# Kernel optimization log

Hardware: AMD Instinct MI355X
Metric: run time of the kernel (lower is better)

Reference implementation:

```python
import jax, jax.numpy as jnp
import numpy as np

B = 262144
N_HEADS = 30  # sum_{n=1..4} n^2
D_SHARED1, D_SHARED2, D_HEAD = 128, 64, 32


def setup_inputs() -> dict:
    key = jax.random.key(0)
    ks = jax.random.split(key, 12)
    x = jax.random.normal(ks[0], (B, 2), dtype=jnp.float32)
    # quantum numbers with validity constraints: 1<=n<=4, 0<=l<n, -l<=m<=l
    n = jax.random.randint(ks[1], (B,), 1, 5, dtype=jnp.int32)
    u1 = jax.random.uniform(ks[2], (B,))
    l = jnp.minimum(jnp.floor(u1 * n).astype(jnp.int32), n - 1)
    u2 = jax.random.uniform(ks[3], (B,))
    m = jnp.clip(jnp.floor(u2 * (2 * l + 1)).astype(jnp.int32) - l, -l, l)
    # shared MLP params (torch Linear -> y = x @ W + b with W stored [in,out] here)
    def xavier(k, shape):
        fan_in, fan_out = shape[-2], shape[-1]
        lim = np.sqrt(6.0 / (fan_in + fan_out)).astype(np.float32)
        return jax.random.uniform(k, shape, jnp.float32, -lim, lim)
    W1s = xavier(ks[4], (2, D_SHARED1))
    b1s = jnp.zeros((D_SHARED1,), jnp.float32)
    W2s = xavier(ks[5], (D_SHARED1, D_SHARED2))
    b2s = jnp.zeros((D_SHARED2,), jnp.float32)
    # stacked expert head params, flat head index = (n-1)n(2n-1)/6 + l^2 + (m+l)
    HW1 = xavier(ks[6], (N_HEADS, D_SHARED2, D_HEAD))
    Hb1 = jnp.zeros((N_HEADS, D_HEAD), jnp.float32)
    HW2 = xavier(ks[7], (N_HEADS, D_HEAD, 2))
    Hb2 = jnp.zeros((N_HEADS, 2), jnp.float32)
    return dict(x=x, n=n, l=l, m=m, W1s=W1s, b1s=b1s, W2s=W2s, b2s=b2s,
                HW1=HW1, Hb1=Hb1, HW2=HW2, Hb2=Hb2)


def reference(x, n, l, m, W1s, b1s, W2s, b2s, HW1, Hb1, HW2, Hb2):
    # shared MLP (dropout is identity in eval mode)
    h = jnp.tanh(x @ W1s + b1s)          # [B,128]
    h = jnp.tanh(h @ W2s + b2s)          # [B,64]
    # flat head id: cumulative squares offset + l^2 + (m+l)
    hid = (n - 1) * n * (2 * n - 1) // 6 + l * l + (m + l)   # [B] in [0,30)
    # per-sample dispatched tiny MLP via gathered weights (grouped batched matvec)
    z = jnp.tanh(jnp.einsum('bi,bio->bo', h, HW1[hid]) + Hb1[hid])   # [B,32]
    out = jnp.einsum('bi,bio->bo', z, HW2[hid]) + Hb2[hid]           # [B,2]
    return out  # [:,0] real part, [:,1] imag part
```

## Files before the change

kernel.cpp:

```cpp
#include <hip/hip_runtime.h>
#include <hip/hip_bf16.h>
#include <math.h>

#define B_TOTAL 262144
#define NHEADS  30
#define D1      128
#define D2      64
#define DH      32
#define BLK     256
#define NBLK_IN (B_TOTAL / BLK)
#define SB      128
#define MAX_MB  (B_TOTAL / SB + NHEADS)

#define TANH_K  2.885390081777927f

typedef __attribute__((ext_vector_type(8))) __bf16 bf16x8;
typedef __attribute__((ext_vector_type(4))) float  f32x4;


__device__ __forceinline__ int head_id(int nn, int ll, int mm) {
    return (nn - 1) * nn * (2 * nn - 1) / 6 + ll * ll + (mm + ll);
}

__device__ __forceinline__ float tanh_pre(float u) {
    float e = __builtin_amdgcn_exp2f(u);
    return 1.0f - 2.0f * __builtin_amdgcn_rcpf(e + 1.0f);
}

__global__ __launch_bounds__(BLK) void k_hist(const int* __restrict__ n,
                                              const int* __restrict__ l,
                                              const int* __restrict__ m,
                                              unsigned* __restrict__ block_counts,
                                              unsigned char* __restrict__ hids,
                                              const float* __restrict__ W2,
                                              const float* __restrict__ HW1,
                                              __bf16* __restrict__ W2f,
                                              __bf16* __restrict__ HW1f) {
    __shared__ unsigned lh[NHEADS];
    int t = threadIdx.x;
    if (t < NHEADS) lh[t] = 0u;
    __syncthreads();
    int i = blockIdx.x * BLK + t;
    int hid = head_id(n[i], l[i], m[i]);
    hids[i] = (unsigned char)hid;
    atomicAdd(&lh[hid], 1u);

    if (blockIdx.x < 272) {
        int idx = blockIdx.x * BLK + t;
        if (idx < 8192) {
            int jj = idx & 7, ln = (idx >> 3) & 63, nt = (idx >> 9) & 3, kt = (idx >> 11) & 3;
            int k = kt * 32 + (ln >> 4) * 8 + jj;
            int c = nt * 16 + (ln & 15);
            W2f[idx] = (__bf16)(W2[k * D2 + c] * TANH_K);
        } else {
            int id2 = idx - 8192;
            int jj = id2 & 7, ln = (id2 >> 3) & 63;
            int nt2 = (id2 >> 9) & 1, kt2 = (id2 >> 10) & 1, h = id2 >> 11;
            int k = kt2 * 32 + (ln >> 4) * 8 + jj;
            int c = nt2 * 16 + (ln & 15);
            HW1f[h * 2048 + ((kt2 * 2 + nt2) * 64 + ln) * 8 + jj] =
                (__bf16)(HW1[h * (D2 * DH) + k * DH + c] * TANH_K);
        }
    }

    __syncthreads();
    if (t < NHEADS) block_counts[t * NBLK_IN + blockIdx.x] = lh[t];
}

__global__ __launch_bounds__(BLK) void k_scan(const unsigned* __restrict__ block_counts,
                                              unsigned* __restrict__ block_off,
                                              unsigned* __restrict__ counts,
                                              unsigned* __restrict__ starts,
                                              int* __restrict__ block_head) {
    int h = blockIdx.x;
    int t = threadIdx.x;
    if (h < NHEADS) {
        __shared__ unsigned wsum[4];
        int lane = t & 63, wv = t >> 6;
        uint4 v = reinterpret_cast<const uint4*>(block_counts + h * NBLK_IN)[t];
        unsigned tsum = v.x + v.y + v.z + v.w;
        unsigned s = tsum;
        #pragma unroll
        for (int d = 1; d < 64; d <<= 1) {
            unsigned u = __shfl_up(s, d, 64);
            if (lane >= d) s += u;
        }
        if (lane == 63) wsum[wv] = s;
        __syncthreads();
        unsigned woff = 0;
        #pragma unroll
        for (int w = 0; w < 3; ++w) woff += (w < wv) ? wsum[w] : 0u;
        unsigned ex = woff + s - tsum;
        uint4 o;
        o.x = ex;
        o.y = ex + v.x;
        o.z = ex + v.x + v.y;
        o.w = ex + v.x + v.y + v.z;
        reinterpret_cast<uint4*>(block_off + h * NBLK_IN)[t] = o;
    } else {
        __shared__ unsigned stotal[NHEADS];
        __shared__ unsigned cumblk[NHEADS + 1];
        int lane = t & 63, wv = t >> 6;
        for (int hh = wv; hh < NHEADS; hh += 4) {
            const uint4* p = reinterpret_cast<const uint4*>(block_counts + hh * NBLK_IN);
            unsigned sum = 0;
            #pragma unroll
            for (int c = 0; c < 4; ++c) {
                uint4 v = p[lane + c * 64];
                sum += v.x + v.y + v.z + v.w;
            }
            #pragma unroll
            for (int d = 32; d >= 1; d >>= 1) sum += __shfl_down(sum, d, 64);
            if (lane == 0) { stotal[hh] = sum; counts[hh] = sum; }
        }
        __syncthreads();
        if (t == 0) {
            unsigned tb = 0;
            for (int hh = 0; hh < NHEADS; ++hh) {
                starts[hh] = tb * SB;
                cumblk[hh] = tb;
                tb += (stotal[hh] + SB - 1) / SB;
            }
            cumblk[NHEADS] = tb;
        }
        __syncthreads();
        unsigned tb = cumblk[NHEADS];
        for (int b = t; b < MAX_MB; b += BLK) {
            int hh = -1;
            if ((unsigned)b < tb) {
                hh = 0;
                while (cumblk[hh + 1] <= (unsigned)b) ++hh;
            }
            block_head[b] = hh;
        }
    }
}

__global__ __launch_bounds__(BLK) void k_scatter(const unsigned char* __restrict__ hids,
                                                 const unsigned* __restrict__ starts,
                                                 const unsigned* __restrict__ block_off,
                                                 int* __restrict__ perm) {
    __shared__ unsigned lcur[NHEADS];
    int t = threadIdx.x;
    if (t < NHEADS) lcur[t] = 0u;
    __syncthreads();
    int i = blockIdx.x * BLK + t;
    int hid = hids[i];
    unsigned rank = atomicAdd(&lcur[hid], 1u);
    unsigned pos = starts[hid] + block_off[hid * NBLK_IN + blockIdx.x] + rank;
    perm[pos] = i;
}

__global__ __launch_bounds__(BLK) void k_main(
    const float* __restrict__ x,
    const float* __restrict__ W1, const float* __restrict__ b1,
    const float* __restrict__ b2,
    const float* __restrict__ Hb1, const float* __restrict__ HW2,
    const float* __restrict__ Hb2,
    const __bf16* __restrict__ W2f, const __bf16* __restrict__ HW1f,
    const int* __restrict__ block_head, const int* __restrict__ perm,
    const unsigned* __restrict__ starts, const unsigned* __restrict__ counts,
    float* __restrict__ out)
{
    int h = block_head[blockIdx.x];
    if (h < 0) return;
    h = __builtin_amdgcn_readfirstlane(h);

    __shared__ float  sW1[3 * D1];
    __shared__ __bf16 T[4][32 * 64];

    int t = threadIdx.x;
    for (int i = t; i < 3 * D1; i += BLK) {
        float v = (i < 2 * D1) ? W1[i] : b1[i - 2 * D1];
        sW1[i] = v * TANH_K;
    }
    __syncthreads();

    int lane = t & 63, wv = t >> 6;
    int kgrp = lane >> 4;
    int lid  = lane & 15;
    int row  = lane & 31;
    int slot = blockIdx.x * SB + wv * 32 + row;
    bool valid = (unsigned)(slot - starts[h]) < counts[h];
    int gi = 0;
    float x0 = 0.f, x1 = 0.f;
    if (valid) {
        gi = perm[slot];
        x0 = x[gi * 2];
        x1 = x[gi * 2 + 1];
    }

    float xs0[2], xs1[2];
    #pragma unroll
    for (int tm = 0; tm < 2; ++tm) {
        int src = tm * 16 + lid;
        xs0[tm] = __shfl(x0, src, 64);
        xs1[tm] = __shfl(x1, src, 64);
    }

    f32x4 acc2[2][4];
    #pragma unroll
    for (int nt = 0; nt < 4; ++nt) {
        float bv = b2[nt * 16 + lid] * TANH_K;
        f32x4 c4 = {bv, bv, bv, bv};
        acc2[0][nt] = c4;
        acc2[1][nt] = c4;
    }

    #pragma unroll
    for (int kt = 0; kt < 4; ++kt) {
        int jb = kt * 32 + kgrp * 8;
        float4 w0a = *(const float4*)&sW1[jb];
        float4 w0b = *(const float4*)&sW1[jb + 4];
        float4 w1a = *(const float4*)&sW1[D1 + jb];
        float4 w1b = *(const float4*)&sW1[D1 + jb + 4];
        float4 bba = *(const float4*)&sW1[2 * D1 + jb];
        float4 bbb = *(const float4*)&sW1[2 * D1 + jb + 4];
        float w0[8] = {w0a.x, w0a.y, w0a.z, w0a.w, w0b.x, w0b.y, w0b.z, w0b.w};
        float w1[8] = {w1a.x, w1a.y, w1a.z, w1a.w, w1b.x, w1b.y, w1b.z, w1b.w};
        float bb[8] = {bba.x, bba.y, bba.z, bba.w, bbb.x, bbb.y, bbb.z, bbb.w};
        bf16x8 a1[2];
        #pragma unroll
        for (int tm = 0; tm < 2; ++tm)
            #pragma unroll
            for (int jj = 0; jj < 8; ++jj) {
                float v = tanh_pre(fmaf(xs1[tm], w1[jj], fmaf(xs0[tm], w0[jj], bb[jj])));
                a1[tm][jj] = (__bf16)v;
            }
        #pragma unroll
        for (int nt = 0; nt < 4; ++nt) {
            bf16x8 bfr = *reinterpret_cast<const bf16x8*>(W2f + ((kt * 4 + nt) * 64 + lane) * 8);
            #pragma unroll
            for (int tm = 0; tm < 2; ++tm)
                acc2[tm][nt] = __builtin_amdgcn_mfma_f32_16x16x32_bf16(a1[tm], bfr, acc2[tm][nt], 0, 0, 0);
        }
    }

    __bf16* Tw = T[wv];
    #pragma unroll
    for (int tm = 0; tm < 2; ++tm)
        #pragma unroll
        for (int nt = 0; nt < 4; ++nt)
            #pragma unroll
            for (int rg = 0; rg < 4; ++rg) {
                int r = tm * 16 + kgrp * 4 + rg;
                int c = nt * 16 + lid;
                int chunk = (c >> 3) ^ (r & 7);
                Tw[r * 64 + chunk * 8 + (c & 7)] = (__bf16)tanh_pre(acc2[tm][nt][rg]);
            }

    f32x4 acc3[2][2];
    #pragma unroll
    for (int nt = 0; nt < 2; ++nt) {
        float bv = Hb1[h * DH + nt * 16 + lid] * TANH_K;
        f32x4 c4 = {bv, bv, bv, bv};
        acc3[0][nt] = c4;
        acc3[1][nt] = c4;
    }
    #pragma unroll
    for (int kt2 = 0; kt2 < 2; ++kt2) {
        #pragma unroll
        for (int tm = 0; tm < 2; ++tm) {
            int r = tm * 16 + lid;
            int chunk = (kt2 * 4 + kgrp) ^ (r & 7);
            bf16x8 a2v = *reinterpret_cast<const bf16x8*>(&Tw[r * 64 + chunk * 8]);
            #pragma unroll
            for (int nt3 = 0; nt3 < 2; ++nt3) {
                bf16x8 bfr = *reinterpret_cast<const bf16x8*>(HW1f + h * 2048 + ((kt2 * 2 + nt3) * 64 + lane) * 8);
                acc3[tm][nt3] = __builtin_amdgcn_mfma_f32_16x16x32_bf16(a2v, bfr, acc3[tm][nt3], 0, 0, 0);
            }
        }
    }

    #pragma unroll
    for (int tm = 0; tm < 2; ++tm)
        #pragma unroll
        for (int nt3 = 0; nt3 < 2; ++nt3)
            #pragma unroll
            for (int rg = 0; rg < 4; ++rg) {
                int r = tm * 16 + kgrp * 4 + rg;
                int c = 32 + nt3 * 16 + lid;
                int chunk = (c >> 3) ^ (r & 7);
                Tw[r * 64 + chunk * 8 + (c & 7)] = (__bf16)tanh_pre(acc3[tm][nt3][rg]);
            }

    const float* hw2 = HW2 + h * DH * 2;
    float o0 = Hb2[h * 2], o1 = Hb2[h * 2 + 1];
    #pragma unroll
    for (int i4 = 0; i4 < 4; ++i4) {
        int chunk = (4 + i4) ^ (row & 7);
        bf16x8 zz = *reinterpret_cast<const bf16x8*>(&Tw[row * 64 + chunk * 8]);
        #pragma unroll
        for (int jj = 0; jj < 8; ++jj) {
            float zv = (float)zz[jj];
            int j = i4 * 8 + jj;
            o0 = fmaf(zv, hw2[2 * j], o0);
            o1 = fmaf(zv, hw2[2 * j + 1], o1);
        }
    }
    if (valid && lane < 32) {
        float2 ov = {o0, o1};
        reinterpret_cast<float2*>(out)[gi] = ov;
    }
}

extern "C" void kernel_launch(void* const* d_in, const int* in_sizes, int n_in,
                              void* d_out, int out_size, void* d_ws, size_t ws_size,
                              hipStream_t stream) {
    const float* x   = (const float*)d_in[0];
    const int*   n   = (const int*)d_in[1];
    const int*   l   = (const int*)d_in[2];
    const int*   m   = (const int*)d_in[3];
    const float* W1  = (const float*)d_in[4];
    const float* b1  = (const float*)d_in[5];
    const float* W2  = (const float*)d_in[6];
    const float* b2  = (const float*)d_in[7];
    const float* HW1 = (const float*)d_in[8];
    const float* Hb1 = (const float*)d_in[9];
    const float* HW2 = (const float*)d_in[10];
    const float* Hb2 = (const float*)d_in[11];
    float* out = (float*)d_out;

    char* ws = (char*)d_ws;
    unsigned* counts       = (unsigned*)(ws + 0);
    unsigned* starts       = (unsigned*)(ws + 128);
    int*      block_head   = (int*)(ws + 512);
    unsigned* block_counts = (unsigned*)(ws + 16384);
    unsigned* block_off    = (unsigned*)(ws + 139264);
    int*      perm         = (int*)(ws + 270336);
    __bf16*   W2f          = (__bf16*)(ws + 4558848);
    __bf16*   HW1f         = (__bf16*)(ws + 4575232);
    unsigned char* hids    = (unsigned char*)(ws + 4700160);

    k_hist   <<<NBLK_IN, BLK, 0, stream>>>(n, l, m, block_counts, hids, W2, HW1, W2f, HW1f);
    k_scan   <<<NHEADS + 1, BLK, 0, stream>>>(block_counts, block_off, counts, starts, block_head);
    k_scatter<<<NBLK_IN, BLK, 0, stream>>>(hids, starts, block_off, perm);
    k_main   <<<MAX_MB, BLK, 0, stream>>>(x, W1, b1, b2, Hb1, HW2, Hb2,
                                          W2f, HW1f, block_head, perm,
                                          starts, counts, out);
}
```

Before: 46.32 us.

## Process two microblocks per workgroup to amortize setup and prefetch inputs

```diff
diff --git a/kernel.cpp b/kernel.cpp
--- a/kernel.cpp
+++ b/kernel.cpp
@@ -11,6 +11,7 @@
 #define NBLK_IN (B_TOTAL / BLK)
 #define SB      128
 #define MAX_MB  (B_TOTAL / SB + NHEADS)
+#define MB2     (MAX_MB / 2)
 
 #define TANH_K  2.885390081777927f
 
@@ -151,44 +152,17 @@
     perm[pos] = i;
 }
 
-__global__ __launch_bounds__(BLK) void k_main(
-    const float* __restrict__ x,
-    const float* __restrict__ W1, const float* __restrict__ b1,
-    const float* __restrict__ b2,
-    const float* __restrict__ Hb1, const float* __restrict__ HW2,
-    const float* __restrict__ Hb2,
+__device__ __forceinline__ void compute_tile(
+    float x0, float x1, int h, int lane, bool valid, int gi,
+    const float* __restrict__ b2, const float* __restrict__ Hb1,
+    const float* __restrict__ HW2, const float* __restrict__ Hb2,
     const __bf16* __restrict__ W2f, const __bf16* __restrict__ HW1f,
-    const int* __restrict__ block_head, const int* __restrict__ perm,
-    const unsigned* __restrict__ starts, const unsigned* __restrict__ counts,
+    const float* __restrict__ sW1, __bf16* __restrict__ Tw,
     float* __restrict__ out)
 {
-    int h = block_head[blockIdx.x];
-    if (h < 0) return;
-    h = __builtin_amdgcn_readfirstlane(h);
-
-    __shared__ float  sW1[3 * D1];
-    __shared__ __bf16 T[4][32 * 64];
-
-    int t = threadIdx.x;
-    for (int i = t; i < 3 * D1; i += BLK) {
-        float v = (i < 2 * D1) ? W1[i] : b1[i - 2 * D1];
-        sW1[i] = v * TANH_K;
-    }
-    __syncthreads();
-
-    int lane = t & 63, wv = t >> 6;
     int kgrp = lane >> 4;
     int lid  = lane & 15;
     int row  = lane & 31;
-    int slot = blockIdx.x * SB + wv * 32 + row;
-    bool valid = (unsigned)(slot - starts[h]) < counts[h];
-    int gi = 0;
-    float x0 = 0.f, x1 = 0.f;
-    if (valid) {
-        gi = perm[slot];
-        x0 = x[gi * 2];
-        x1 = x[gi * 2 + 1];
-    }
 
     float xs0[2], xs1[2];
     #pragma unroll
@@ -236,7 +210,6 @@
         }
     }
 
-    __bf16* Tw = T[wv];
     #pragma unroll
     for (int tm = 0; tm < 2; ++tm)
         #pragma unroll
@@ -301,6 +274,69 @@
     if (valid && lane < 32) {
         float2 ov = {o0, o1};
         reinterpret_cast<float2*>(out)[gi] = ov;
+    }
+}
+
+__global__ __launch_bounds__(BLK, 3) void k_main(
+    const float* __restrict__ x,
+    const float* __restrict__ W1, const float* __restrict__ b1,
+    const float* __restrict__ b2,
+    const float* __restrict__ Hb1, const float* __restrict__ HW2,
+    const float* __restrict__ Hb2,
+    const __bf16* __restrict__ W2f, const __bf16* __restrict__ HW1f,
+    const int* __restrict__ block_head, const int* __restrict__ perm,
+    const unsigned* __restrict__ starts, const unsigned* __restrict__ counts,
+    float* __restrict__ out)
+{
+    int mb0 = blockIdx.x * 2;
+    int mb1 = mb0 + 1;
+    int h0 = block_head[mb0];
+    int h1 = block_head[mb1];
+    if (h0 < 0) return;
+
+    __shared__ float  sW1[3 * D1];
+    __shared__ __bf16 T[4][32 * 64];
+
+    int t = threadIdx.x;
+    for (int i = t; i < 3 * D1; i += BLK) {
+        float v = (i < 2 * D1) ? W1[i] : b1[i - 2 * D1];
+        sW1[i] = v * TANH_K;
+    }
+
+    int lane = t & 63, wv = t >> 6;
+    int row  = lane & 31;
+
+    h0 = __builtin_amdgcn_readfirstlane(h0);
+    int slot0 = mb0 * SB + wv * 32 + row;
+    bool valid0 = (unsigned)(slot0 - starts[h0]) < counts[h0];
+    int gi0 = 0; float x00 = 0.f, x10 = 0.f;
+    if (valid0) {
+        gi0 = perm[slot0];
+        x00 = x[gi0 * 2];
+        x10 = x[gi0 * 2 + 1];
+    }
+    bool have1 = h1 >= 0;
+    int h1u = have1 ? __builtin_amdgcn_readfirstlane(h1) : 0;
+    int gi1 = 0; float x01 = 0.f, x11 = 0.f;
+    bool valid1 = false;
+    if (have1) {
+        int slot1 = mb1 * SB + wv * 32 + row;
+        valid1 = (unsigned)(slot1 - starts[h1u]) < counts[h1u];
+        if (valid1) {
+            gi1 = perm[slot1];
+            x01 = x[gi1 * 2];
+            x11 = x[gi1 * 2 + 1];
+        }
+    }
+    __syncthreads();
+
+    __bf16* Tw = T[wv];
+    compute_tile(x00, x10, h0, lane, valid0, gi0,
+                 b2, Hb1, HW2, Hb2, W2f, HW1f, sW1, Tw, out);
+    if (have1) {
+        asm volatile("s_waitcnt lgkmcnt(0)" ::: "memory");
+        compute_tile(x01, x11, h1u, lane, valid1, gi1,
+                     b2, Hb1, HW2, Hb2, W2f, HW1f, sW1, Tw, out);
     }
 }
 
@@ -335,7 +371,7 @@
     k_hist   <<<NBLK_IN, BLK, 0, stream>>>(n, l, m, block_counts, hids, W2, HW1, W2f, HW1f);
     k_scan   <<<NHEADS + 1, BLK, 0, stream>>>(block_counts, block_off, counts, starts, block_head);
     k_scatter<<<NBLK_IN, BLK, 0, stream>>>(hids, starts, block_off, perm);
-    k_main   <<<MAX_MB, BLK, 0, stream>>>(x, W1, b1, b2, Hb1, HW2, Hb2,
-                                          W2f, HW1f, block_head, perm,
-                                          starts, counts, out);
-}
+    k_main   <<<MB2, BLK, 0, stream>>>(x, W1, b1, b2, Hb1, HW2, Hb2,
+                                       W2f, HW1f, block_head, perm,
+                                       starts, counts, out);
+}
```

Result: slower. 48.72 us (+5.2%).

## Precompute in-block ranks in histogram and pre-permute x during scatter

Applied to the files above, without the earlier changes.

```diff
diff --git a/kernel.cpp b/kernel.cpp
--- a/kernel.cpp
+++ b/kernel.cpp
@@ -32,6 +32,7 @@
                                               const int* __restrict__ m,
                                               unsigned* __restrict__ block_counts,
                                               unsigned char* __restrict__ hids,
+                                              unsigned char* __restrict__ ranks,
                                               const float* __restrict__ W2,
                                               const float* __restrict__ HW1,
                                               __bf16* __restrict__ W2f,
@@ -42,8 +43,9 @@
     __syncthreads();
     int i = blockIdx.x * BLK + t;
     int hid = head_id(n[i], l[i], m[i]);
-    hids[i] = (unsigned char)hid;
-    atomicAdd(&lh[hid], 1u);
+    unsigned rank = atomicAdd(&lh[hid], 1u);
+    hids[i]  = (unsigned char)hid;
+    ranks[i] = (unsigned char)rank;
 
     if (blockIdx.x < 272) {
         int idx = blockIdx.x * BLK + t;
@@ -137,22 +139,23 @@
 }
 
 __global__ __launch_bounds__(BLK) void k_scatter(const unsigned char* __restrict__ hids,
+                                                 const unsigned char* __restrict__ ranks,
+                                                 const float* __restrict__ x,
                                                  const unsigned* __restrict__ starts,
                                                  const unsigned* __restrict__ block_off,
-                                                 int* __restrict__ perm) {
-    __shared__ unsigned lcur[NHEADS];
-    int t = threadIdx.x;
-    if (t < NHEADS) lcur[t] = 0u;
-    __syncthreads();
-    int i = blockIdx.x * BLK + t;
-    int hid = hids[i];
-    unsigned rank = atomicAdd(&lcur[hid], 1u);
+                                                 int* __restrict__ perm,
+                                                 float2* __restrict__ xs) {
+    int i = blockIdx.x * BLK + threadIdx.x;
+    int hid  = hids[i];
+    int rank = ranks[i];
     unsigned pos = starts[hid] + block_off[hid * NBLK_IN + blockIdx.x] + rank;
+    float2 xv = reinterpret_cast<const float2*>(x)[i];
     perm[pos] = i;
+    xs[pos]   = xv;
 }
 
 __global__ __launch_bounds__(BLK) void k_main(
-    const float* __restrict__ x,
+    const float2* __restrict__ xs,
     const float* __restrict__ W1, const float* __restrict__ b1,
     const float* __restrict__ b2,
     const float* __restrict__ Hb1, const float* __restrict__ HW2,
@@ -186,8 +189,9 @@
     float x0 = 0.f, x1 = 0.f;
     if (valid) {
         gi = perm[slot];
-        x0 = x[gi * 2];
-        x1 = x[gi * 2 + 1];
+        float2 xv = xs[slot];
+        x0 = xv.x;
+        x1 = xv.y;
     }
 
     float xs0[2], xs1[2];
@@ -328,14 +332,17 @@
     unsigned* block_counts = (unsigned*)(ws + 16384);
     unsigned* block_off    = (unsigned*)(ws + 139264);
     int*      perm         = (int*)(ws + 270336);
+    float2*   xs           = (float2*)(ws + 1349632);
+    unsigned char* ranks   = (unsigned char*)(ws + 3477504);
     __bf16*   W2f          = (__bf16*)(ws + 4558848);
     __bf16*   HW1f         = (__bf16*)(ws + 4575232);
     unsigned char* hids    = (unsigned char*)(ws + 4700160);
 
-    k_hist   <<<NBLK_IN, BLK, 0, stream>>>(n, l, m, block_counts, hids, W2, HW1, W2f, HW1f);
+    k_hist   <<<NBLK_IN, BLK, 0, stream>>>(n, l, m, block_counts, hids, ranks,
+                                           W2, HW1, W2f, HW1f);
     k_scan   <<<NHEADS + 1, BLK, 0, stream>>>(block_counts, block_off, counts, starts, block_head);
-    k_scatter<<<NBLK_IN, BLK, 0, stream>>>(hids, starts, block_off, perm);
-    k_main   <<<MAX_MB, BLK, 0, stream>>>(x, W1, b1, b2, Hb1, HW2, Hb2,
+    k_scatter<<<NBLK_IN, BLK, 0, stream>>>(hids, ranks, x, starts, block_off, perm, xs);
+    k_main   <<<MAX_MB, BLK, 0, stream>>>(xs, W1, b1, b2, Hb1, HW2, Hb2,
                                           W2f, HW1f, block_head, perm,
                                           starts, counts, out);
 }
```

After: 47.49 us. 2.5% more time.
